# Kernel optimization log

Hardware: AMD Instinct MI355X
Metric: run time of the kernel (lower is better)

Reference implementation:

```python
import jax, jax.numpy as jnp
import numpy as np

DK, DV, NH = 512, 256, 8  # matches init_kwargs


def rel_to_abs(x):
    # x: (B, N, L, 2L-1) -> (B, N, L, L) via pad/reshape trick
    B, N, L, _ = x.shape
    x = jnp.pad(x, ((0, 0), (0, 0), (0, 0), (0, 1)))          # (B,N,L,2L)
    x = x.reshape(B, N, L * 2 * L)
    x = jnp.pad(x, ((0, 0), (0, 0), (0, L - 1)))
    x = x.reshape(B, N, L + 1, 2 * L - 1)
    return x[:, :, :L, L - 1:]


def relative_logits_1d(q, rel_k):
    # q: (B, nh, A, Wd, dkh); rel_k: (dkh, 2*Wd-1)
    B, nh, A, Wd, _ = q.shape
    rel = jnp.einsum('bnawc,cm->bnawm', q, rel_k)             # (B,nh,A,Wd,2Wd-1)
    rel = rel.reshape(B, nh * A, Wd, 2 * Wd - 1)
    rel = rel_to_abs(rel).reshape(B, nh, A, 1, Wd, Wd)
    return jnp.broadcast_to(rel, (B, nh, A, A, Wd, Wd))


def reference(x, w_qkv, w_conv, w_out, key_rel_h, key_rel_w):
    B, Cin, H, W = x.shape
    dkh, dvh = DK // NH, DV // NH
    L = H * W
    # 1x1 qkv projection (stride 1)
    qkv = jnp.einsum('bchw,oc->bohw', x, w_qkv)               # (B, 2dk+dv, H, W)
    q = qkv[:, :DK]
    k = qkv[:, DK:2 * DK]
    v = qkv[:, 2 * DK:]
    flat_q = q.reshape(B, NH, dkh, L) * (dkh ** -0.5)
    flat_k = k.reshape(B, NH, dkh, L)
    flat_v = v.reshape(B, NH, dvh, L)
    logits = jnp.einsum('bncs,bnct->bnst', flat_q, flat_k)     # (B,nh,L,L)
    # relative position logits (uses the already-scaled q, as in the torch code)
    qr = flat_q.reshape(B, NH, dkh, H, W).transpose(0, 1, 3, 4, 2)  # (B,nh,H,W,dkh)
    w_rel = relative_logits_1d(qr, key_rel_w)                  # (B,nh,H,H,W,W)
    h_rel = relative_logits_1d(qr.transpose(0, 1, 3, 2, 4), key_rel_h)  # (B,nh,W,W,H,H)
    h_rel = h_rel.transpose(0, 1, 2, 4, 3, 5).reshape(B, NH, L, L)
    w_rel = w_rel.transpose(0, 1, 4, 2, 5, 3).reshape(B, NH, L, L)
    logits = logits + h_rel + w_rel
    weights = jax.nn.softmax(logits, axis=-1)
    attn = jnp.einsum('bnst,bnct->bnsc', weights, flat_v)      # (B,nh,L,dvh)
    attn = attn.transpose(0, 1, 3, 2).reshape(B, DV, H, W)
    attn = jnp.einsum('bchw,oc->bohw', attn, w_out)            # 1x1 out_proj
    conv_out = jax.lax.conv_general_dilated(
        x, w_conv, window_strides=(1, 1), padding=[(1, 1), (1, 1)],
        dimension_numbers=('NCHW', 'OIHW', 'NCHW'))            # (B, out_c-dv, H, W)
    return jnp.concatenate([conv_out, attn], axis=1)


def setup_inputs() -> dict:
    key = jax.random.key(0)
    ks = jax.random.split(key, 6)
    H, W, Cin = 32, 32, 256
    return {
        'x': jax.random.normal(ks[0], (8, Cin, H, W), jnp.float32),
        'w_qkv': jax.random.normal(ks[1], (2 * DK + DV, Cin), jnp.float32) * 0.02,
        'w_conv': jax.random.normal(ks[2], (256, Cin, 3, 3), jnp.float32) * 0.02,
        'w_out': jax.random.normal(ks[3], (DV, DV), jnp.float32) * 0.02,
        'key_rel_h': DK ** -0.5 + jax.random.normal(ks[4], (DK // NH, 2 * H - 1), jnp.float32),
        'key_rel_w': DK ** -0.5 + jax.random.normal(ks[5], (DK // NH, 2 * W - 1), jnp.float32),
    }
```

## Files before the change

### kernel.cpp

```cpp
#include <hip/hip_runtime.h>
#include <cstddef>
#include <cstdint>

#define NB 8
#define CIN 256
#define LL 1024
#define DKC 512
#define DVC 256
#define XPSTRIDE 295936

typedef short short8 __attribute__((ext_vector_type(8)));
typedef float f32x4 __attribute__((ext_vector_type(4)));

__device__ __forceinline__ unsigned short f2bf(float f) {
  unsigned int u = __float_as_uint(f);
  u += 0x7fffu + ((u >> 16) & 1u);
  return (unsigned short)(u >> 16);
}
__device__ __forceinline__ float bf2f(unsigned short u) {
  return __uint_as_float(((unsigned int)u) << 16);
}

__global__ __launch_bounds__(256) void prep_weights(
    const float* __restrict__ wconv, const float* __restrict__ wqkv,
    const float* __restrict__ wout, const float* __restrict__ krh,
    const float* __restrict__ krw, unsigned short* __restrict__ wtap,
    unsigned short* __restrict__ wqbf, unsigned short* __restrict__ woutbf,
    unsigned short* __restrict__ relTh, unsigned short* __restrict__ relTw) {
  const int idx = blockIdx.x * 256 + threadIdx.x;
  if (idx < 589824) {
    const int tap = idx >> 16;
    const int rem = idx & 65535;
    wtap[idx] = f2bf(wconv[(size_t)rem * 9 + tap]);
  } else if (idx < 917504) {
    const int j = idx - 589824;
    const int o = j >> 8;
    const float sc = (o < DKC) ? 0.125f * 1.44269504088896f : 1.0f;
    wqbf[j] = f2bf(wqkv[j] * sc);
  } else if (idx < 983040) {
    const int j = idx - 917504;
    woutbf[j] = f2bf(wout[j]);
  } else {
    const int j = idx - 983040;
    const int tbl = j >> 12;
    const int rest = j & 4095;
    const int m = rest >> 6, c = rest & 63;
    const float* src = tbl ? krw : krh;
    unsigned short* dst = tbl ? relTw : relTh;
    const float v = (m < 63) ? src[c * 63 + m] : 0.f;
    dst[m * 64 + c] = f2bf(v);
  }
}

__global__ __launch_bounds__(256) void xpad_border(unsigned short* __restrict__ xTp) {
  const int idx = blockIdx.x * 256 + threadIdx.x;
  const int b = idx / 33792;
  const int rem = idx - b * 33792;
  const int pos = rem >> 8, c = rem & 255;
  int hp, wp;
  if (pos < 34) { hp = 0; wp = pos; }
  else if (pos < 68) { hp = 33; wp = pos - 34; }
  else if (pos < 100) { hp = pos - 68 + 1; wp = 0; }
  else { hp = pos - 100 + 1; wp = 33; }
  xTp[(size_t)b * XPSTRIDE + (hp * 34 + wp) * 256 + c] = 0;
}

__global__ __launch_bounds__(256) void xpad_interior(
    const float* __restrict__ x, unsigned short* __restrict__ xTp) {
  __shared__ float tile[64][65];
  const int st = blockIdx.x;
  const int b = blockIdx.y;
  const int s0 = st * 64;
  const int h0 = st * 2;
  const int tid = threadIdx.x;
  for (int cc = 0; cc < 4; ++cc) {
    const int c0 = cc * 64;
    {
      const int row = tid >> 2;
      const int j0 = (tid & 3) * 16;
#pragma unroll
      for (int k = 0; k < 4; ++k)
        *(float4*)&tile[row][j0 + k * 4] =
            *(const float4*)(x + ((size_t)(b * CIN + c0 + row)) * LL + s0 + j0 + k * 4);
    }
    __syncthreads();
    {
      const int sl = tid >> 2;
      const int cb = (tid & 3) * 16;
      unsigned short buf[16];
#pragma unroll
      for (int m = 0; m < 16; ++m) buf[m] = f2bf(tile[cb + m][sl]);
      const int hp = h0 + (sl >> 5) + 1;
      const int wp = (sl & 31) + 1;
      unsigned short* dst = xTp + (size_t)b * XPSTRIDE + (hp * 34 + wp) * 256 + c0 + cb;
      *(uint4*)dst = *(uint4*)&buf[0];
      *(uint4*)(dst + 8) = *(uint4*)&buf[8];
    }
    __syncthreads();
  }
}

__global__ __launch_bounds__(256) void qkv_mfma(
    const unsigned short* __restrict__ xTp, const unsigned short* __restrict__ wqbf,
    unsigned short* __restrict__ qbf, unsigned short* __restrict__ kbf,
    unsigned short* __restrict__ vbf) {
  __shared__ __align__(16) unsigned short as[64 * 64];
  __shared__ __align__(16) unsigned short bs[64 * 64];
  __shared__ float trans[64][65];
  const int tid = threadIdx.x;
  const int lane = tid & 63, w = tid >> 6;
  const int n16 = lane & 15, quad = lane >> 4;
  const int ot = blockIdx.x;
  const int st = blockIdx.y;
  const int b = blockIdx.z;
  const int o0 = ot * 64;
  const int s0 = st * 64;
  const int h0 = st * 2;
  const int trow = tid >> 3, ck = tid & 7;

  const unsigned short* xb = xTp + (size_t)b * XPSTRIDE;
  const unsigned short* wt = wqbf + (size_t)o0 * 256;
  const int wpos = (trow & 31) + 1;

  f32x4 acc[4];
#pragma unroll
  for (int nt = 0; nt < 4; ++nt) acc[nt] = (f32x4){0.f, 0.f, 0.f, 0.f};

  uint4 ra0, ra1, rb0, rb1;
  {
    ra0 = *(const uint4*)(wt + (size_t)trow * 256 + ck * 8);
    ra1 = *(const uint4*)(wt + (size_t)(trow + 32) * 256 + ck * 8);
    rb0 = *(const uint4*)(xb + (size_t)((h0 + 1) * 34 + wpos) * 256 + ck * 8);
    rb1 = *(const uint4*)(xb + (size_t)((h0 + 2) * 34 + wpos) * 256 + ck * 8);
  }
#pragma unroll
  for (int kc = 0; kc < 4; ++kc) {
    __syncthreads();
    *(uint4*)&as[trow * 64 + ((ck ^ (trow & 7)) * 8)] = ra0;
    *(uint4*)&as[(trow + 32) * 64 + ((ck ^ (trow & 7)) * 8)] = ra1;
    *(uint4*)&bs[trow * 64 + ((ck ^ (trow & 7)) * 8)] = rb0;
    *(uint4*)&bs[(trow + 32) * 64 + ((ck ^ (trow & 7)) * 8)] = rb1;
    __syncthreads();
    if (kc < 3) {
      const int c0 = (kc + 1) * 64;
      ra0 = *(const uint4*)(wt + (size_t)trow * 256 + c0 + ck * 8);
      ra1 = *(const uint4*)(wt + (size_t)(trow + 32) * 256 + c0 + ck * 8);
      rb0 = *(const uint4*)(xb + (size_t)((h0 + 1) * 34 + wpos) * 256 + c0 + ck * 8);
      rb1 = *(const uint4*)(xb + (size_t)((h0 + 2) * 34 + wpos) * 256 + c0 + ck * 8);
    }
    short8 a0 = *(const short8*)&as[(w * 16 + n16) * 64 + ((quad ^ (n16 & 7)) * 8)];
    short8 a1 = *(const short8*)&as[(w * 16 + n16) * 64 + (((quad + 4) ^ (n16 & 7)) * 8)];
#pragma unroll
    for (int nt = 0; nt < 4; ++nt) {
      short8 b0 = *(const short8*)&bs[(nt * 16 + n16) * 64 + ((quad ^ (n16 & 7)) * 8)];
      short8 b1 = *(const short8*)&bs[(nt * 16 + n16) * 64 + (((quad + 4) ^ (n16 & 7)) * 8)];
      acc[nt] = __builtin_amdgcn_mfma_f32_16x16x32_bf16(a0, b0, acc[nt], 0, 0, 0);
      acc[nt] = __builtin_amdgcn_mfma_f32_16x16x32_bf16(a1, b1, acc[nt], 0, 0, 0);
    }
  }
  __syncthreads();
#pragma unroll
  for (int nt = 0; nt < 4; ++nt)
#pragma unroll
    for (int reg = 0; reg < 4; ++reg)
      trans[w * 16 + quad * 4 + reg][nt * 16 + n16] = acc[nt][reg];
  __syncthreads();
  const int sl = tid >> 2;
  const int cseg = (tid & 3) * 16;
  unsigned short buf[16];
  if (ot < 16) {
#pragma unroll
    for (int m = 0; m < 16; ++m) buf[m] = f2bf(trans[cseg + m][sl]);
    unsigned short* dst;
    int head;
    if (ot < 8) { dst = qbf; head = ot; }
    else { dst = kbf; head = ot - 8; }
    const size_t base = (((size_t)(b * 8 + head)) * LL + s0 + sl) * 64 + cseg;
    *(uint4*)(dst + base) = *(uint4*)&buf[0];
    *(uint4*)(dst + base + 8) = *(uint4*)&buf[8];
  } else {
#pragma unroll
    for (int m = 0; m < 16; ++m) buf[m] = f2bf(trans[sl][cseg + m]);
    unsigned short* dst = vbf + ((size_t)b * DVC + (ot - 16) * 64 + sl) * LL + s0 + cseg;
    *(uint4*)dst = *(uint4*)&buf[0];
    *(uint4*)(dst + 8) = *(uint4*)&buf[8];
  }
}

__global__ __launch_bounds__(256) void conv_mfma(
    const unsigned short* __restrict__ xTp, const unsigned short* __restrict__ wtap,
    float* __restrict__ out) {
  __shared__ __align__(16) unsigned short as[64 * 64];
  __shared__ __align__(16) unsigned short bs[64 * 64];
  const int tid = threadIdx.x;
  const int lane = tid & 63, w = tid >> 6;
  const int n16 = lane & 15, quad = lane >> 4;
  const int ot = blockIdx.x;
  const int st = blockIdx.y;
  const int b = blockIdx.z;
  const int s0 = st * 64;
  const int h0 = st * 2;
  const int trow = tid >> 3;
  const int ck = tid & 7;

  const unsigned short* xb = xTp + (size_t)b * XPSTRIDE;
  const unsigned short* wbase = wtap + (size_t)(ot * 64) * 256;

  f32x4 acc[4];
#pragma unroll
  for (int nt = 0; nt < 4; ++nt) acc[nt] = (f32x4){0.f, 0.f, 0.f, 0.f};

  uint4 ra0, ra1, rb0, rb1;
  auto loadtile = [&](int it) {
    const int tap = it >> 2;
    const int c0 = (it & 3) * 64;
    const int dh = tap / 3 - 1;
    const int dw = tap - (tap / 3) * 3 - 1;
    const unsigned short* wt = wbase + (size_t)tap * 65536;
    ra0 = *(const uint4*)(wt + (size_t)trow * 256 + c0 + ck * 8);
    ra1 = *(const uint4*)(wt + (size_t)(trow + 32) * 256 + c0 + ck * 8);
    const int wp = (trow & 31) + dw + 1;
    rb0 = *(const uint4*)(xb + (size_t)((h0 + dh + 1) * 34 + wp) * 256 + c0 + ck * 8);
    rb1 = *(const uint4*)(xb + (size_t)((h0 + dh + 2) * 34 + wp) * 256 + c0 + ck * 8);
  };
  loadtile(0);
  for (int it = 0; it < 36; ++it) {
    __syncthreads();
    *(uint4*)&as[trow * 64 + ((ck ^ (trow & 7)) * 8)] = ra0;
    *(uint4*)&as[(trow + 32) * 64 + ((ck ^ (trow & 7)) * 8)] = ra1;
    *(uint4*)&bs[trow * 64 + ((ck ^ (trow & 7)) * 8)] = rb0;
    *(uint4*)&bs[(trow + 32) * 64 + ((ck ^ (trow & 7)) * 8)] = rb1;
    __syncthreads();
    if (it < 35) loadtile(it + 1);
    short8 a0 = *(const short8*)&as[(w * 16 + n16) * 64 + ((quad ^ (n16 & 7)) * 8)];
    short8 a1 = *(const short8*)&as[(w * 16 + n16) * 64 + (((quad + 4) ^ (n16 & 7)) * 8)];
#pragma unroll
    for (int nt = 0; nt < 4; ++nt) {
      short8 b0 = *(const short8*)&bs[(nt * 16 + n16) * 64 + ((quad ^ (n16 & 7)) * 8)];
      short8 b1 = *(const short8*)&bs[(nt * 16 + n16) * 64 + (((quad + 4) ^ (n16 & 7)) * 8)];
      acc[nt] = __builtin_amdgcn_mfma_f32_16x16x32_bf16(a0, b0, acc[nt], 0, 0, 0);
      acc[nt] = __builtin_amdgcn_mfma_f32_16x16x32_bf16(a1, b1, acc[nt], 0, 0, 0);
    }
  }
#pragma unroll
  for (int nt = 0; nt < 4; ++nt)
#pragma unroll
    for (int reg = 0; reg < 4; ++reg)
      out[((size_t)b * 512 + ot * 64 + w * 16 + quad * 4 + reg) * LL + s0 + nt * 16 + n16] =
          acc[nt][reg];
}

__global__ __launch_bounds__(256, 4) void attn_kernel(
    const unsigned short* __restrict__ qbf, const unsigned short* __restrict__ kbf,
    const unsigned short* __restrict__ vbf, const unsigned short* __restrict__ relTh,
    const unsigned short* __restrict__ relTw, unsigned short* __restrict__ abf) {
  __shared__ __align__(16) char smem[28672];
  unsigned short* ks = (unsigned short*)smem;
  unsigned short* vs = (unsigned short*)(smem + 8192);
  unsigned short* ps = (unsigned short*)(smem + 12288);
  unsigned short* rwtT = (unsigned short*)(smem + 20480);
  float* obuf = (float*)smem;

  const int tid = threadIdx.x;
  const int lane = tid & 63, w = tid >> 6;
  const int n16 = lane & 15, quad = lane >> 4;
  const int blk = blockIdx.x;
  const int bn = blk & 63, qb = blk >> 6;
  const int n = bn & 7, b = bn >> 3;
  const int s0 = qb * 64;
  const int aa = 2 * qb + (w >> 1);
  const int pb = (w & 1) * 16;

  const unsigned short* qbase = qbf + ((size_t)(b * 8 + n)) * LL * 64;
  const unsigned short* kbase = kbf + ((size_t)(b * 8 + n)) * LL * 64;
  const unsigned short* vbase = vbf + ((size_t)(b * 8 + n)) * 32 * LL;

  const int ck = tid & 7;
  const int trow = tid >> 3;

  uint4 pk0 = *(const uint4*)(kbase + trow * 64 + ck * 8);
  uint4 pk1 = *(const uint4*)(kbase + (trow + 32) * 64 + ck * 8);
  uint4 pv = *(const uint4*)(vbase + (size_t)trow * LL + ck * 8);

  {
    const int sT = (pb + n16) * 32 + aa;
    short8 ra0 = *(const short8*)(qbase + (size_t)sT * 64 + quad * 8);
    short8 ra1 = *(const short8*)(qbase + (size_t)sT * 64 + 32 + quad * 8);
#pragma unroll
    for (int tbl = 0; tbl < 2; ++tbl) {
      const unsigned short* rel = tbl ? relTh : relTw;
      f32x4 acc[4];
#pragma unroll
      for (int mt = 0; mt < 4; ++mt) acc[mt] = (f32x4){0.f, 0.f, 0.f, 0.f};
#pragma unroll
      for (int mt = 0; mt < 4; ++mt) {
        short8 b0 = *(const short8*)(rel + (mt * 16 + n16) * 64 + quad * 8);
        short8 b1 = *(const short8*)(rel + (mt * 16 + n16) * 64 + 32 + quad * 8);
        acc[mt] = __builtin_amdgcn_mfma_f32_16x16x32_bf16(ra0, b0, acc[mt], 0, 0, 0);
        acc[mt] = __builtin_amdgcn_mfma_f32_16x16x32_bf16(ra1, b1, acc[mt], 0, 0, 0);
      }
      if (tbl == 0) {
#pragma unroll
        for (int mt = 0; mt < 4; ++mt)
#pragma unroll
          for (int reg = 0; reg < 4; ++reg)
            rwtT[(mt * 16 + n16) * 64 +
                 ((w * 16 + quad * 4 + reg) ^ ((n16 & 7) * 8))] = f2bf(acc[mt][reg]);
      } else {
#pragma unroll
        for (int mt = 0; mt < 4; ++mt)
#pragma unroll
          for (int reg = 0; reg < 4; ++reg)
            ps[(w * 16 + quad * 4 + reg) * 64 + mt * 16 + n16] = f2bf(acc[mt][reg]);
      }
    }
  }
  short8 qf0 = *(const short8*)(qbase + (size_t)(s0 + w * 16 + n16) * 64 + quad * 8);
  short8 qf1 = *(const short8*)(qbase + (size_t)(s0 + w * 16 + n16) * 64 + 32 + quad * 8);
  __syncthreads();
  float rhreg[2][4];
#pragma unroll
  for (int tt1 = 0; tt1 < 2; ++tt1)
#pragma unroll
    for (int reg = 0; reg < 4; ++reg) {
      const int iL = quad * 4 + reg;
      rhreg[tt1][reg] = bf2f(ps[(w * 16 + iL) * 64 + tt1 * 16 + n16 + 31 - pb - iL]);
    }

  float lacc[4] = {0.f, 0.f, 0.f, 0.f};
  f32x4 oacc[2];
  oacc[0] = (f32x4){0.f, 0.f, 0.f, 0.f};
  oacc[1] = (f32x4){0.f, 0.f, 0.f, 0.f};

  unsigned short* psw = ps + w * 1024;
  const int rb = w * 16 + quad * 4;

  for (int kt64 = 0; kt64 < 16; ++kt64) {
    const int t0 = kt64 * 64;
    __syncthreads();
    *(uint4*)&ks[trow * 64 + ((ck ^ (trow & 7)) * 8)] = pk0;
    *(uint4*)&ks[(trow + 32) * 64 + ((ck ^ (trow & 7)) * 8)] = pk1;
    *(uint4*)&vs[trow * 64 + ((ck ^ (trow & 7)) * 8)] = pv;
    __syncthreads();
    if (kt64 < 15) {
      const unsigned short* kg = kbase + (size_t)(t0 + 64) * 64;
      pk0 = *(const uint4*)(kg + trow * 64 + ck * 8);
      pk1 = *(const uint4*)(kg + (trow + 32) * 64 + ck * 8);
      pv = *(const uint4*)(vbase + (size_t)trow * LL + t0 + 64 + ck * 8);
    }

    f32x4 sacc[4];
#pragma unroll
    for (int tt = 0; tt < 4; ++tt) sacc[tt] = (f32x4){0.f, 0.f, 0.f, 0.f};
#pragma unroll
    for (int tt = 0; tt < 4; ++tt) {
      short8 kb0 = *(const short8*)&ks[(tt * 16 + n16) * 64 + ((quad ^ (n16 & 7)) * 8)];
      short8 kb1 = *(const short8*)&ks[(tt * 16 + n16) * 64 + (((quad + 4) ^ (n16 & 7)) * 8)];
      sacc[tt] = __builtin_amdgcn_mfma_f32_16x16x32_bf16(qf0, kb0, sacc[tt], 0, 0, 0);
      sacc[tt] = __builtin_amdgcn_mfma_f32_16x16x32_bf16(qf1, kb1, sacc[tt], 0, 0, 0);
    }
    float rwv[2][4];
#pragma unroll
    for (int h = 0; h < 2; ++h) {
      const int mw = (t0 >> 5) + h - aa + 31;
      const ushort4 rw4 = *(const ushort4*)&rwtT[mw * 64 + (rb ^ ((mw & 7) * 8))];
      rwv[h][0] = bf2f(rw4.x); rwv[h][1] = bf2f(rw4.y);
      rwv[h][2] = bf2f(rw4.z); rwv[h][3] = bf2f(rw4.w);
    }
#pragma unroll
    for (int tt = 0; tt < 4; ++tt)
#pragma unroll
      for (int reg = 0; reg < 4; ++reg) {
        const float e =
            __builtin_amdgcn_exp2f(sacc[tt][reg] + rwv[tt >> 1][reg] + rhreg[tt & 1][reg]);
        lacc[reg] += e;
        const int r = quad * 4 + reg;
        psw[r * 64 + (((tt * 2 + (n16 >> 3)) ^ (r & 7)) * 8) + (n16 & 7)] =
            (unsigned short)(__float_as_uint(e) >> 16);
      }
    __asm__ volatile("s_waitcnt lgkmcnt(0)" ::: "memory");
#pragma unroll
    for (int kt = 0; kt < 2; ++kt) {
      short8 pa = *(const short8*)&psw[n16 * 64 + (((quad + 4 * kt) ^ (n16 & 7)) * 8)];
#pragma unroll
      for (int ct = 0; ct < 2; ++ct) {
        short8 vb = *(const short8*)&vs[(ct * 16 + n16) * 64 + (((quad + 4 * kt) ^ (n16 & 7)) * 8)];
        oacc[ct] = __builtin_amdgcn_mfma_f32_16x16x32_bf16(pa, vb, oacc[ct], 0, 0, 0);
      }
    }
  }
  float linv[4];
#pragma unroll
  for (int reg = 0; reg < 4; ++reg) {
    float l = lacc[reg];
#pragma unroll
    for (int m = 1; m < 16; m <<= 1) l += __shfl_xor(l, m, 16);
    linv[reg] = 1.0f / l;
  }
  __syncthreads();
#pragma unroll
  for (int ct = 0; ct < 2; ++ct)
#pragma unroll
    for (int reg = 0; reg < 4; ++reg)
      obuf[(w * 16 + quad * 4 + reg) * 33 + ct * 16 + n16] = oacc[ct][reg] * linv[reg];
  __syncthreads();
  {
    const int row = tid >> 2;
    const int cseg = (tid & 3) * 8;
    unsigned short buf8[8];
#pragma unroll
    for (int m = 0; m < 8; ++m) buf8[m] = f2bf(obuf[row * 33 + cseg + m]);
    *(uint4*)(abf + (((size_t)b * LL) + s0 + row) * 256 + n * 32 + cseg) = *(uint4*)&buf8[0];
  }
}

__global__ __launch_bounds__(256) void proj_mfma(
    const unsigned short* __restrict__ abf, const unsigned short* __restrict__ woutbf,
    float* __restrict__ out) {
  __shared__ __align__(16) unsigned short as[64 * 64];
  __shared__ __align__(16) unsigned short bs[64 * 64];
  const int tid = threadIdx.x;
  const int lane = tid & 63, w = tid >> 6;
  const int n16 = lane & 15, quad = lane >> 4;
  const int ot = blockIdx.x;
  const int st = blockIdx.y;
  const int b = blockIdx.z;
  const int o0 = ot * 64;
  const int s0 = st * 64;
  const int trow = tid >> 3, ck = tid & 7;

  const unsigned short* ab = abf + ((size_t)b * LL + s0) * 256;
  const unsigned short* wt = woutbf + (size_t)o0 * 256;

  f32x4 acc[4];
#pragma unroll
  for (int nt = 0; nt < 4; ++nt) acc[nt] = (f32x4){0.f, 0.f, 0.f, 0.f};

  uint4 ra0, ra1, rb0, rb1;
  ra0 = *(const uint4*)(wt + (size_t)trow * 256 + ck * 8);
  ra1 = *(const uint4*)(wt + (size_t)(trow + 32) * 256 + ck * 8);
  rb0 = *(const uint4*)(ab + (size_t)trow * 256 + ck * 8);
  rb1 = *(const uint4*)(ab + (size_t)(trow + 32) * 256 + ck * 8);
#pragma unroll
  for (int kc = 0; kc < 4; ++kc) {
    __syncthreads();
    *(uint4*)&as[trow * 64 + ((ck ^ (trow & 7)) * 8)] = ra0;
    *(uint4*)&as[(trow + 32) * 64 + ((ck ^ (trow & 7)) * 8)] = ra1;
    *(uint4*)&bs[trow * 64 + ((ck ^ (trow & 7)) * 8)] = rb0;
    *(uint4*)&bs[(trow + 32) * 64 + ((ck ^ (trow & 7)) * 8)] = rb1;
    __syncthreads();
    if (kc < 3) {
      const int c0 = (kc + 1) * 64;
      ra0 = *(const uint4*)(wt + (size_t)trow * 256 + c0 + ck * 8);
      ra1 = *(const uint4*)(wt + (size_t)(trow + 32) * 256 + c0 + ck * 8);
      rb0 = *(const uint4*)(ab + (size_t)trow * 256 + c0 + ck * 8);
      rb1 = *(const uint4*)(ab + (size_t)(trow + 32) * 256 + c0 + ck * 8);
    }
    short8 a0 = *(const short8*)&as[(w * 16 + n16) * 64 + ((quad ^ (n16 & 7)) * 8)];
    short8 a1 = *(const short8*)&as[(w * 16 + n16) * 64 + (((quad + 4) ^ (n16 & 7)) * 8)];
#pragma unroll
    for (int nt = 0; nt < 4; ++nt) {
      short8 b0 = *(const short8*)&bs[(nt * 16 + n16) * 64 + ((quad ^ (n16 & 7)) * 8)];
      short8 b1 = *(const short8*)&bs[(nt * 16 + n16) * 64 + (((quad + 4) ^ (n16 & 7)) * 8)];
      acc[nt] = __builtin_amdgcn_mfma_f32_16x16x32_bf16(a0, b0, acc[nt], 0, 0, 0);
      acc[nt] = __builtin_amdgcn_mfma_f32_16x16x32_bf16(a1, b1, acc[nt], 0, 0, 0);
    }
  }
#pragma unroll
  for (int nt = 0; nt < 4; ++nt)
#pragma unroll
    for (int reg = 0; reg < 4; ++reg)
      out[((size_t)b * 512 + 256 + o0 + w * 16 + quad * 4 + reg) * LL + s0 + nt * 16 + n16] =
          acc[nt][reg];
}

extern "C" void kernel_launch(void* const* d_in, const int* in_sizes, int n_in,
                              void* d_out, int out_size, void* d_ws, size_t ws_size,
                              hipStream_t stream) {
  const float* x     = (const float*)d_in[0];
  const float* wqkv  = (const float*)d_in[1];
  const float* wconv = (const float*)d_in[2];
  const float* wout  = (const float*)d_in[3];
  const float* krh   = (const float*)d_in[4];
  const float* krw   = (const float*)d_in[5];
  float* out = (float*)d_out;

  unsigned short* qbf = (unsigned short*)d_ws;
  unsigned short* kbf = qbf + (size_t)NB * 8 * LL * 64;
  unsigned short* vbf = kbf + (size_t)NB * 8 * LL * 64;
  unsigned short* abf = vbf + (size_t)NB * DVC * LL;
  unsigned short* relTh = abf + (size_t)NB * LL * DVC;
  unsigned short* relTw = relTh + 4096;
  unsigned short* xTp = relTw + 4096;
  unsigned short* wtap = xTp + (size_t)NB * XPSTRIDE;
  unsigned short* wqbf = wtap + 589824;
  unsigned short* woutbf = wqbf + 327680;

  prep_weights<<<dim3(3872), 256, 0, stream>>>(wconv, wqkv, wout, krh, krw,
                                               wtap, wqbf, woutbf, relTh, relTw);
  xpad_border<<<dim3(1056), 256, 0, stream>>>(xTp);
  xpad_interior<<<dim3(16, 8), 256, 0, stream>>>(x, xTp);
  qkv_mfma<<<dim3(20, 16, NB), 256, 0, stream>>>(xTp, wqbf, qbf, kbf, vbf);
  conv_mfma<<<dim3(4, 16, NB), 256, 0, stream>>>(xTp, wtap, out);
  attn_kernel<<<dim3(1024), 256, 0, stream>>>(qbf, kbf, vbf, relTh, relTw, abf);
  proj_mfma<<<dim3(4, 16, NB), 256, 0, stream>>>(abf, woutbf, out);
}
```

Measured before the change: 160.8 us.

## Pre-tile weights into MFMA fragment order and load A operands directly from global

Weight prep now writes conv, qkv and out-projection weights in a blocked 64x64 tile layout, so each lane can load its MFMA A fragment straight from global memory. The A-tile LDS staging, its shared-memory footprint and the LDS reads are removed from qkv_mfma, conv_mfma and proj_mfma. The padded-input border zeroing is folded into the prep_weights launch, so one kernel launch is dropped. The trade-off is direct global loads for the A fragments, which depend on L2 locality and are only prefetched one step ahead.

```diff
diff --git a/kernel.cpp b/kernel.cpp
--- a/kernel.cpp
+++ b/kernel.cpp
@@ -26,21 +26,32 @@
     const float* __restrict__ wout, const float* __restrict__ krh,
     const float* __restrict__ krw, unsigned short* __restrict__ wtap,
     unsigned short* __restrict__ wqbf, unsigned short* __restrict__ woutbf,
-    unsigned short* __restrict__ relTh, unsigned short* __restrict__ relTw) {
+    unsigned short* __restrict__ relTh, unsigned short* __restrict__ relTw,
+    unsigned short* __restrict__ xTp) {
   const int idx = blockIdx.x * 256 + threadIdx.x;
   if (idx < 589824) {
-    const int tap = idx >> 16;
-    const int rem = idx & 65535;
-    wtap[idx] = f2bf(wconv[(size_t)rem * 9 + tap]);
+    const int g = idx >> 14;
+    const int ot = g / 9, tap = g - ot * 9;
+    const int rem2 = idx & 16383;
+    const int kc = rem2 >> 12;
+    const int row = (rem2 >> 6) & 63, kin = rem2 & 63;
+    const int o = ot * 64 + row, c = kc * 64 + kin;
+    wtap[idx] = f2bf(wconv[(size_t)(o * 256 + c) * 9 + tap]);
   } else if (idx < 917504) {
     const int j = idx - 589824;
-    const int o = j >> 8;
+    const int g = j >> 12;
+    const int ot = g >> 2, kc = g & 3;
+    const int row = (j >> 6) & 63, kin = j & 63;
+    const int o = ot * 64 + row, c = kc * 64 + kin;
     const float sc = (o < DKC) ? 0.125f * 1.44269504088896f : 1.0f;
-    wqbf[j] = f2bf(wqkv[j] * sc);
+    wqbf[j] = f2bf(wqkv[o * 256 + c] * sc);
   } else if (idx < 983040) {
     const int j = idx - 917504;
-    woutbf[j] = f2bf(wout[j]);
-  } else {
+    const int g = j >> 12;
+    const int o = (g >> 2) * 64 + ((j >> 6) & 63);
+    const int c = (g & 3) * 64 + (j & 63);
+    woutbf[j] = f2bf(wout[o * 256 + c]);
+  } else if (idx < 991232) {
     const int j = idx - 983040;
     const int tbl = j >> 12;
     const int rest = j & 4095;
@@ -49,20 +60,18 @@
     unsigned short* dst = tbl ? relTw : relTh;
     const float v = (m < 63) ? src[c * 63 + m] : 0.f;
     dst[m * 64 + c] = f2bf(v);
-  }
-}
-
-__global__ __launch_bounds__(256) void xpad_border(unsigned short* __restrict__ xTp) {
-  const int idx = blockIdx.x * 256 + threadIdx.x;
-  const int b = idx / 33792;
-  const int rem = idx - b * 33792;
-  const int pos = rem >> 8, c = rem & 255;
-  int hp, wp;
-  if (pos < 34) { hp = 0; wp = pos; }
-  else if (pos < 68) { hp = 33; wp = pos - 34; }
-  else if (pos < 100) { hp = pos - 68 + 1; wp = 0; }
-  else { hp = pos - 100 + 1; wp = 33; }
-  xTp[(size_t)b * XPSTRIDE + (hp * 34 + wp) * 256 + c] = 0;
+  } else {
+    const int j2 = idx - 991232;
+    const int b = j2 / 33792;
+    const int rem = j2 - b * 33792;
+    const int pos = rem >> 8, c = rem & 255;
+    int hp, wp;
+    if (pos < 34) { hp = 0; wp = pos; }
+    else if (pos < 68) { hp = 33; wp = pos - 34; }
+    else if (pos < 100) { hp = pos - 68 + 1; wp = 0; }
+    else { hp = pos - 100 + 1; wp = 33; }
+    xTp[(size_t)b * XPSTRIDE + (hp * 34 + wp) * 256 + c] = 0;
+  }
 }
 
 __global__ __launch_bounds__(256) void xpad_interior(
@@ -104,52 +113,45 @@
     const unsigned short* __restrict__ xTp, const unsigned short* __restrict__ wqbf,
     unsigned short* __restrict__ qbf, unsigned short* __restrict__ kbf,
     unsigned short* __restrict__ vbf) {
-  __shared__ __align__(16) unsigned short as[64 * 64];
-  __shared__ __align__(16) unsigned short bs[64 * 64];
-  __shared__ float trans[64][65];
+  __shared__ __align__(16) char qsmem[16640];
+  unsigned short* bs = (unsigned short*)qsmem;
+  float (*trans)[65] = (float(*)[65])qsmem;
   const int tid = threadIdx.x;
   const int lane = tid & 63, w = tid >> 6;
   const int n16 = lane & 15, quad = lane >> 4;
   const int ot = blockIdx.x;
   const int st = blockIdx.y;
   const int b = blockIdx.z;
-  const int o0 = ot * 64;
   const int s0 = st * 64;
   const int h0 = st * 2;
   const int trow = tid >> 3, ck = tid & 7;
 
   const unsigned short* xb = xTp + (size_t)b * XPSTRIDE;
-  const unsigned short* wt = wqbf + (size_t)o0 * 256;
+  const unsigned short* wA = wqbf + (size_t)ot * 16384 + (w * 16 + n16) * 64 + quad * 8;
   const int wpos = (trow & 31) + 1;
 
   f32x4 acc[4];
 #pragma unroll
   for (int nt = 0; nt < 4; ++nt) acc[nt] = (f32x4){0.f, 0.f, 0.f, 0.f};
 
-  uint4 ra0, ra1, rb0, rb1;
-  {
-    ra0 = *(const uint4*)(wt + (size_t)trow * 256 + ck * 8);
-    ra1 = *(const uint4*)(wt + (size_t)(trow + 32) * 256 + ck * 8);
-    rb0 = *(const uint4*)(xb + (size_t)((h0 + 1) * 34 + wpos) * 256 + ck * 8);
-    rb1 = *(const uint4*)(xb + (size_t)((h0 + 2) * 34 + wpos) * 256 + ck * 8);
-  }
+  uint4 rb0 = *(const uint4*)(xb + (size_t)((h0 + 1) * 34 + wpos) * 256 + ck * 8);
+  uint4 rb1 = *(const uint4*)(xb + (size_t)((h0 + 2) * 34 + wpos) * 256 + ck * 8);
+  short8 af0 = *(const short8*)(wA);
+  short8 af1 = *(const short8*)(wA + 32);
 #pragma unroll
   for (int kc = 0; kc < 4; ++kc) {
     __syncthreads();
-    *(uint4*)&as[trow * 64 + ((ck ^ (trow & 7)) * 8)] = ra0;
-    *(uint4*)&as[(trow + 32) * 64 + ((ck ^ (trow & 7)) * 8)] = ra1;
     *(uint4*)&bs[trow * 64 + ((ck ^ (trow & 7)) * 8)] = rb0;
     *(uint4*)&bs[(trow + 32) * 64 + ((ck ^ (trow & 7)) * 8)] = rb1;
     __syncthreads();
+    short8 a0 = af0, a1 = af1;
     if (kc < 3) {
       const int c0 = (kc + 1) * 64;
-      ra0 = *(const uint4*)(wt + (size_t)trow * 256 + c0 + ck * 8);
-      ra1 = *(const uint4*)(wt + (size_t)(trow + 32) * 256 + c0 + ck * 8);
       rb0 = *(const uint4*)(xb + (size_t)((h0 + 1) * 34 + wpos) * 256 + c0 + ck * 8);
       rb1 = *(const uint4*)(xb + (size_t)((h0 + 2) * 34 + wpos) * 256 + c0 + ck * 8);
-    }
-    short8 a0 = *(const short8*)&as[(w * 16 + n16) * 64 + ((quad ^ (n16 & 7)) * 8)];
-    short8 a1 = *(const short8*)&as[(w * 16 + n16) * 64 + (((quad + 4) ^ (n16 & 7)) * 8)];
+      af0 = *(const short8*)(wA + (kc + 1) * 4096);
+      af1 = *(const short8*)(wA + (kc + 1) * 4096 + 32);
+    }
 #pragma unroll
     for (int nt = 0; nt < 4; ++nt) {
       short8 b0 = *(const short8*)&bs[(nt * 16 + n16) * 64 + ((quad ^ (n16 & 7)) * 8)];
@@ -190,7 +192,6 @@
 __global__ __launch_bounds__(256) void conv_mfma(
     const unsigned short* __restrict__ xTp, const unsigned short* __restrict__ wtap,
     float* __restrict__ out) {
-  __shared__ __align__(16) unsigned short as[64 * 64];
   __shared__ __align__(16) unsigned short bs[64 * 64];
   const int tid = threadIdx.x;
   const int lane = tid & 63, w = tid >> 6;
@@ -204,36 +205,36 @@
   const int ck = tid & 7;
 
   const unsigned short* xb = xTp + (size_t)b * XPSTRIDE;
-  const unsigned short* wbase = wtap + (size_t)(ot * 64) * 256;
+  const unsigned short* wA = wtap + (size_t)ot * 147456 + (w * 16 + n16) * 64 + quad * 8;
 
   f32x4 acc[4];
 #pragma unroll
   for (int nt = 0; nt < 4; ++nt) acc[nt] = (f32x4){0.f, 0.f, 0.f, 0.f};
 
-  uint4 ra0, ra1, rb0, rb1;
-  auto loadtile = [&](int it) {
+  uint4 rb0, rb1;
+  auto loadB = [&](int it) {
     const int tap = it >> 2;
     const int c0 = (it & 3) * 64;
     const int dh = tap / 3 - 1;
     const int dw = tap - (tap / 3) * 3 - 1;
-    const unsigned short* wt = wbase + (size_t)tap * 65536;
-    ra0 = *(const uint4*)(wt + (size_t)trow * 256 + c0 + ck * 8);
-    ra1 = *(const uint4*)(wt + (size_t)(trow + 32) * 256 + c0 + ck * 8);
     const int wp = (trow & 31) + dw + 1;
     rb0 = *(const uint4*)(xb + (size_t)((h0 + dh + 1) * 34 + wp) * 256 + c0 + ck * 8);
     rb1 = *(const uint4*)(xb + (size_t)((h0 + dh + 2) * 34 + wp) * 256 + c0 + ck * 8);
   };
-  loadtile(0);
+  loadB(0);
+  short8 af0 = *(const short8*)(wA);
+  short8 af1 = *(const short8*)(wA + 32);
   for (int it = 0; it < 36; ++it) {
     __syncthreads();
-    *(uint4*)&as[trow * 64 + ((ck ^ (trow & 7)) * 8)] = ra0;
-    *(uint4*)&as[(trow + 32) * 64 + ((ck ^ (trow & 7)) * 8)] = ra1;
     *(uint4*)&bs[trow * 64 + ((ck ^ (trow & 7)) * 8)] = rb0;
     *(uint4*)&bs[(trow + 32) * 64 + ((ck ^ (trow & 7)) * 8)] = rb1;
     __syncthreads();
-    if (it < 35) loadtile(it + 1);
-    short8 a0 = *(const short8*)&as[(w * 16 + n16) * 64 + ((quad ^ (n16 & 7)) * 8)];
-    short8 a1 = *(const short8*)&as[(w * 16 + n16) * 64 + (((quad + 4) ^ (n16 & 7)) * 8)];
+    short8 a0 = af0, a1 = af1;
+    if (it < 35) {
+      loadB(it + 1);
+      af0 = *(const short8*)(wA + (size_t)(it + 1) * 4096);
+      af1 = *(const short8*)(wA + (size_t)(it + 1) * 4096 + 32);
+    }
 #pragma unroll
     for (int nt = 0; nt < 4; ++nt) {
       short8 b0 = *(const short8*)&bs[(nt * 16 + n16) * 64 + ((quad ^ (n16 & 7)) * 8)];
@@ -417,7 +418,6 @@
 __global__ __launch_bounds__(256) void proj_mfma(
     const unsigned short* __restrict__ abf, const unsigned short* __restrict__ woutbf,
     float* __restrict__ out) {
-  __shared__ __align__(16) unsigned short as[64 * 64];
   __shared__ __align__(16) unsigned short bs[64 * 64];
   const int tid = threadIdx.x;
   const int lane = tid & 63, w = tid >> 6;
@@ -425,39 +425,34 @@
   const int ot = blockIdx.x;
   const int st = blockIdx.y;
   const int b = blockIdx.z;
-  const int o0 = ot * 64;
   const int s0 = st * 64;
   const int trow = tid >> 3, ck = tid & 7;
 
   const unsigned short* ab = abf + ((size_t)b * LL + s0) * 256;
-  const unsigned short* wt = woutbf + (size_t)o0 * 256;
+  const unsigned short* wA = woutbf + (size_t)ot * 16384 + (w * 16 + n16) * 64 + quad * 8;
 
   f32x4 acc[4];
 #pragma unroll
   for (int nt = 0; nt < 4; ++nt) acc[nt] = (f32x4){0.f, 0.f, 0.f, 0.f};
 
-  uint4 ra0, ra1, rb0, rb1;
-  ra0 = *(const uint4*)(wt + (size_t)trow * 256 + ck * 8);
-  ra1 = *(const uint4*)(wt + (size_t)(trow + 32) * 256 + ck * 8);
-  rb0 = *(const uint4*)(ab + (size_t)trow * 256 + ck * 8);
-  rb1 = *(const uint4*)(ab + (size_t)(trow + 32) * 256 + ck * 8);
+  uint4 rb0 = *(const uint4*)(ab + (size_t)trow * 256 + ck * 8);
+  uint4 rb1 = *(const uint4*)(ab + (size_t)(trow + 32) * 256 + ck * 8);
+  short8 af0 = *(const short8*)(wA);
+  short8 af1 = *(const short8*)(wA + 32);
 #pragma unroll
   for (int kc = 0; kc < 4; ++kc) {
     __syncthreads();
-    *(uint4*)&as[trow * 64 + ((ck ^ (trow & 7)) * 8)] = ra0;
-    *(uint4*)&as[(trow + 32) * 64 + ((ck ^ (trow & 7)) * 8)] = ra1;
     *(uint4*)&bs[trow * 64 + ((ck ^ (trow & 7)) * 8)] = rb0;
     *(uint4*)&bs[(trow + 32) * 64 + ((ck ^ (trow & 7)) * 8)] = rb1;
     __syncthreads();
+    short8 a0 = af0, a1 = af1;
     if (kc < 3) {
       const int c0 = (kc + 1) * 64;
-      ra0 = *(const uint4*)(wt + (size_t)trow * 256 + c0 + ck * 8);
-      ra1 = *(const uint4*)(wt + (size_t)(trow + 32) * 256 + c0 + ck * 8);
       rb0 = *(const uint4*)(ab + (size_t)trow * 256 + c0 + ck * 8);
       rb1 = *(const uint4*)(ab + (size_t)(trow + 32) * 256 + c0 + ck * 8);
-    }
-    short8 a0 = *(const short8*)&as[(w * 16 + n16) * 64 + ((quad ^ (n16 & 7)) * 8)];
-    short8 a1 = *(const short8*)&as[(w * 16 + n16) * 64 + (((quad + 4) ^ (n16 & 7)) * 8)];
+      af0 = *(const short8*)(wA + (kc + 1) * 4096);
+      af1 = *(const short8*)(wA + (kc + 1) * 4096 + 32);
+    }
 #pragma unroll
     for (int nt = 0; nt < 4; ++nt) {
       short8 b0 = *(const short8*)&bs[(nt * 16 + n16) * 64 + ((quad ^ (n16 & 7)) * 8)];
@@ -470,7 +465,7 @@
   for (int nt = 0; nt < 4; ++nt)
 #pragma unroll
     for (int reg = 0; reg < 4; ++reg)
-      out[((size_t)b * 512 + 256 + o0 + w * 16 + quad * 4 + reg) * LL + s0 + nt * 16 + n16] =
+      out[((size_t)b * 512 + 256 + ot * 64 + w * 16 + quad * 4 + reg) * LL + s0 + nt * 16 + n16] =
           acc[nt][reg];
 }
 
@@ -496,9 +491,8 @@
   unsigned short* wqbf = wtap + 589824;
   unsigned short* woutbf = wqbf + 327680;
 
-  prep_weights<<<dim3(3872), 256, 0, stream>>>(wconv, wqkv, wout, krh, krw,
-                                               wtap, wqbf, woutbf, relTh, relTw);
-  xpad_border<<<dim3(1056), 256, 0, stream>>>(xTp);
+  prep_weights<<<dim3(4928), 256, 0, stream>>>(wconv, wqkv, wout, krh, krw,
+                                               wtap, wqbf, woutbf, relTh, relTw, xTp);
   xpad_interior<<<dim3(16, 8), 256, 0, stream>>>(x, xTp);
   qkv_mfma<<<dim3(20, 16, NB), 256, 0, stream>>>(xTp, wqbf, qbf, kbf, vbf);
   conv_mfma<<<dim3(4, 16, NB), 256, 0, stream>>>(xTp, wtap, out);
```

New measurement: 162.7 us. About the same (+1.2%).
